# Performance work log

Hardware: AMD Instinct MI355X
Metric: run time of the kernel (lower is better)

The kernel has to match this reference:

```python
import jax, jax.numpy as jnp
import numpy as np

D_MODEL = 1024
D_HEAD = 64
M_BITS = 32


def setup_inputs() -> dict:
    key = jax.random.key(0)
    ks = jax.random.split(key, 6)
    B, N, M = 2, 2048, 2048
    Q = jax.random.normal(ks[0], (B, N, D_MODEL), dtype=jnp.float32)
    K = jax.random.normal(ks[1], (B, M, D_MODEL), dtype=jnp.float32)
    V = jax.random.normal(ks[2], (B, M, D_MODEL), dtype=jnp.float32)
    s = 1.0 / np.sqrt(D_MODEL)
    Wq = jax.random.normal(ks[3], (D_MODEL, M_BITS), dtype=jnp.float32) * s
    Wk = jax.random.normal(ks[4], (D_MODEL, M_BITS), dtype=jnp.float32) * s
    Wv = jax.random.normal(ks[5], (D_MODEL, D_HEAD), dtype=jnp.float32) * s
    temperature = jnp.ones((1,), dtype=jnp.float32)
    return {"Q": Q, "K": K, "V": V, "Wq": Wq, "Wk": Wk, "Wv": Wv,
            "temperature": temperature}


def tropical_matmul(A, Bt):
    # A: [B, N, m], Bt: [B, M, m] (already transposed form of [B, m, M])
    # (A \odot B)_{ij} = min_k (A_ik + B_kj)
    return jnp.min(A[:, :, None, :] + Bt[:, None, :, :], axis=-1)  # [B, N, M]


def reference(Q, K, V, Wq, Wk, Wv, temperature):
    # REWA tropical encoders (continuous): linear projections to m_bits
    Qt = jnp.einsum('bnd,dm->bnm', Q, Wq)   # [B, N, m_bits]
    Kt = jnp.einsum('bsd,dm->bsm', K, Wk)   # [B, M, m_bits]
    Vp = jnp.einsum('bsd,dh->bsh', V, Wv)   # [B, M, d_head]
    # tropical (min-plus) scores, negated so shorter paths score higher
    scores = -tropical_matmul(Qt, Kt)       # [B, N, M]
    scores = scores / jax.nn.softplus(temperature[0])
    attn = jax.nn.softmax(scores, axis=-1)  # [B, N, M]
    out = jnp.einsum('bnm,bmh->bnh', attn, Vp)  # [B, N, d_head]
    return out, attn
```

## Files before the change

kernel.cpp:

```cpp
#include <hip/hip_runtime.h>
#include <math.h>

#define DM 1024
#define NB 2048
#define MBITS 32
#define DH 64

typedef __attribute__((ext_vector_type(4))) float floatx4;
typedef __attribute__((ext_vector_type(8))) short shortx8;

__device__ __forceinline__ unsigned short f32_to_bf16(float f) {
    union { float f; unsigned u; } v; v.f = f;
    unsigned r = v.u + 0x7FFF + ((v.u >> 16) & 1);
    return (unsigned short)(r >> 16);
}

__device__ __forceinline__ void split2(float x0, float x1, unsigned& hp, unsigned& lp) {
    union { float f; unsigned u; } a, b; a.f = x0; b.f = x1;
    unsigned h0 = a.u & 0xFFFF0000u, h1 = b.u & 0xFFFF0000u;
    union { unsigned u; float f; } hf0, hf1; hf0.u = h0; hf1.u = h1;
    union { float f; unsigned u; } c, d;
    c.f = x0 - hf0.f;
    d.f = x1 - hf1.f;
    hp = (h0 >> 16) | h1;
    lp = (c.u >> 16) | (d.u & 0xFFFF0000u);
}

__global__ __launch_bounds__(256) void wprep_kernel(
    const float* __restrict__ Wq, const float* __restrict__ Wk,
    const float* __restrict__ Wv, unsigned short* __restrict__ Wf)
{
    int wv = blockIdx.x * 4 + (threadIdx.x >> 6);
    int l  = threadIdx.x & 63;
    const float* W; int C, kc32, ct;
    if (wv < 64)       { W = Wq; C = 32; kc32 = wv >> 1;  ct = wv & 1; }
    else if (wv < 128) { W = Wk; C = 32; int z = wv - 64;  kc32 = z >> 1; ct = z & 1; }
    else               { W = Wv; C = 64; int z = wv - 128; kc32 = z >> 2; ct = z & 3; }
    int k0 = kc32 * 32 + (l >> 4) * 8;
    int c  = ct * 16 + (l & 15);
    float x[8];
    #pragma unroll
    for (int j = 0; j < 8; ++j) x[j] = W[(size_t)(k0 + j) * C + c];
    unsigned hp[4], lp[4];
    #pragma unroll
    for (int j2 = 0; j2 < 4; ++j2) split2(x[2 * j2], x[2 * j2 + 1], hp[j2], lp[j2]);
    uint4 hv; hv.x = hp[0]; hv.y = hp[1]; hv.z = hp[2]; hv.w = hp[3];
    uint4 lv; lv.x = lp[0]; lv.y = lp[1]; lv.z = lp[2]; lv.w = lp[3];
    *(uint4*)&Wf[(size_t)wv * 1024 + l * 8]       = hv;
    *(uint4*)&Wf[(size_t)wv * 1024 + 512 + l * 8] = lv;
}

__global__ __launch_bounds__(256) void proj_mfma2_kernel(
    const float* __restrict__ Q, const float* __restrict__ K, const float* __restrict__ V,
    const unsigned short* __restrict__ Wf,
    float* __restrict__ Qt, float* __restrict__ KtT, unsigned short* __restrict__ VpT)
{
    __shared__ float red[4][64][16];

    int gb = blockIdx.x;
    int job = gb >> 8, tile = gb & 255;
    int r0 = tile * 16;
    const float* X = (job == 0) ? Q : (job == 1) ? K : V;
    int ntct  = (job == 2) ? 4 : 2;
    int pbase = job << 6;
    int t = threadIdx.x, w = t >> 6, l = t & 63;
    int lrow = l & 15, lq = l >> 4;

    const float* xrow = &X[(size_t)(r0 + lrow) * DM + w * 256 + lq * 8];

    floatx4 acc[4];
    #pragma unroll
    for (int i = 0; i < 4; ++i) acc[i] = (floatx4){0.f, 0.f, 0.f, 0.f};

    #pragma unroll
    for (int s = 0; s < 8; ++s) {
        floatx4 g0 = *(const floatx4*)(xrow + s * 32);
        floatx4 g1 = *(const floatx4*)(xrow + s * 32 + 4);
        union { unsigned u[4]; shortx8 v; } ahi, alo;
        split2(g0.x, g0.y, ahi.u[0], alo.u[0]);
        split2(g0.z, g0.w, ahi.u[1], alo.u[1]);
        split2(g1.x, g1.y, ahi.u[2], alo.u[2]);
        split2(g1.z, g1.w, ahi.u[3], alo.u[3]);
        int kc32 = w * 8 + s;
        #pragma unroll
        for (int ct = 0; ct < 4; ++ct) {
            if (ct >= ntct) break;
            int p = pbase + kc32 * ntct + ct;
            const unsigned short* wp = &Wf[(size_t)p * 1024 + l * 8];
            shortx8 bhi = *(const shortx8*)wp;
            shortx8 blo = *(const shortx8*)(wp + 512);
            acc[ct] = __builtin_amdgcn_mfma_f32_16x16x32_bf16(ahi.v, bhi, acc[ct], 0, 0, 0);
            acc[ct] = __builtin_amdgcn_mfma_f32_16x16x32_bf16(ahi.v, blo, acc[ct], 0, 0, 0);
            acc[ct] = __builtin_amdgcn_mfma_f32_16x16x32_bf16(alo.v, bhi, acc[ct], 0, 0, 0);
        }
    }

    #pragma unroll
    for (int ct = 0; ct < 4; ++ct) {
        if (ct >= ntct) break;
        #pragma unroll
        for (int r = 0; r < 4; ++r) red[w][l][ct * 4 + r] = acc[ct][r];
    }
    __syncthreads();

    int row = r0 + lq * 4 + w;
    if (job == 0) {
        #pragma unroll
        for (int ct = 0; ct < 2; ++ct) {
            float v = red[0][l][ct * 4 + w] + red[1][l][ct * 4 + w]
                    + red[2][l][ct * 4 + w] + red[3][l][ct * 4 + w];
            Qt[(size_t)row * MBITS + ct * 16 + lrow] = v;
        }
    } else if (job == 1) {
        int bb = row >> 11, j = row & 2047;
        #pragma unroll
        for (int ct = 0; ct < 2; ++ct) {
            float v = red[0][l][ct * 4 + w] + red[1][l][ct * 4 + w]
                    + red[2][l][ct * 4 + w] + red[3][l][ct * 4 + w];
            KtT[(size_t)bb * (MBITS * NB) + (size_t)(ct * 16 + lrow) * NB + j] = v;
        }
    } else {
        int bb = row >> 11, j = row & 2047;
        #pragma unroll
        for (int ct = 0; ct < 4; ++ct) {
            float v = red[0][l][ct * 4 + w] + red[1][l][ct * 4 + w]
                    + red[2][l][ct * 4 + w] + red[3][l][ct * 4 + w];
            VpT[(size_t)bb * (DH * NB) + (size_t)(ct * 16 + lrow) * NB + j] = f32_to_bf16(v);
        }
    }
}

__global__ __launch_bounds__(1024) void fused_score_out_kernel(
    const float* __restrict__ Qt, const float* __restrict__ KtT,
    const unsigned short* __restrict__ VpT, const float* __restrict__ temp,
    float* __restrict__ outp, float* __restrict__ attn)
{
    __shared__ unsigned short Elds[16][2056];
    __shared__ float redsum2[16][2];
    __shared__ float redC[12][64][4];

    const int b  = blockIdx.y;
    const int i0 = blockIdx.x * 8;
    const int t  = threadIdx.x;
    const int w  = t >> 6, l = t & 63;

    {
        uint4 z; z.x = 0; z.y = 0; z.z = 0; z.w = 0;
        uint4* base = (uint4*)&Elds[8][0];
        for (int zi = t; zi < 2056; zi += 1024) base[zi] = z;
    }

    const float tv = temp[0];
    const float c2 = -(1.0f / log1pf(__expf(tv))) * 1.44269504088896340736f;

    {
        const int ip  = w & 3;
        const int jqb = (w >> 2) * 512;
        const int p   = l >> 4;
        const int l16 = l & 15;

        const float* Qbase = &Qt[(size_t)(b * NB + i0 + ip * 2) * MBITS + p * 8];
        floatx4 qa0 = *(const floatx4*)(Qbase);
        floatx4 qa1 = *(const floatx4*)(Qbase + 4);
        floatx4 qb0 = *(const floatx4*)(Qbase + MBITS);
        floatx4 qb1 = *(const floatx4*)(Qbase + MBITS + 4);

        const float* Kp = &KtT[(size_t)b * (MBITS * NB) + (size_t)(p * 8) * NB];
        float sacc0 = 0.f, sacc1 = 0.f;

        #pragma unroll 1
        for (int s = 0; s < 4; ++s) {
            const int j0 = jqb + s * 128 + l16 * 8;
            float m0[8], m1[8];
            #pragma unroll
            for (int jj = 0; jj < 8; ++jj) { m0[jj] = 1e30f; m1[jj] = 1e30f; }

            #pragma unroll
            for (int kp = 0; kp < 8; ++kp) {
                const float* kr = Kp + (size_t)kp * NB + j0;
                floatx4 k0 = *(const floatx4*)kr;
                floatx4 k1 = *(const floatx4*)(kr + 4);
                float qa = (kp < 4) ? qa0[kp] : qa1[kp - 4];
                float qb = (kp < 4) ? qb0[kp] : qb1[kp - 4];
                float kv[8] = {k0.x, k0.y, k0.z, k0.w, k1.x, k1.y, k1.z, k1.w};
                #pragma unroll
                for (int jj = 0; jj < 8; ++jj) {
                    m0[jj] = fminf(m0[jj], qa + kv[jj]);
                    m1[jj] = fminf(m1[jj], qb + kv[jj]);
                }
            }
            #pragma unroll
            for (int jj = 0; jj < 8; ++jj) {
                m0[jj] = fminf(m0[jj], __shfl_xor(m0[jj], 16, 64));
                m0[jj] = fminf(m0[jj], __shfl_xor(m0[jj], 32, 64));
                m1[jj] = fminf(m1[jj], __shfl_xor(m1[jj], 16, 64));
                m1[jj] = fminf(m1[jj], __shfl_xor(m1[jj], 32, 64));
            }
            float e0[8], e1[8];
            #pragma unroll
            for (int jj = 0; jj < 8; ++jj) {
                e0[jj] = exp2f(c2 * m0[jj]);
                e1[jj] = exp2f(c2 * m1[jj]);
            }
            uint4 u0, u1;
            u0.x = (unsigned)f32_to_bf16(e0[0]) | ((unsigned)f32_to_bf16(e0[1]) << 16);
            u0.y = (unsigned)f32_to_bf16(e0[2]) | ((unsigned)f32_to_bf16(e0[3]) << 16);
            u0.z = (unsigned)f32_to_bf16(e0[4]) | ((unsigned)f32_to_bf16(e0[5]) << 16);
            u0.w = (unsigned)f32_to_bf16(e0[6]) | ((unsigned)f32_to_bf16(e0[7]) << 16);
            u1.x = (unsigned)f32_to_bf16(e1[0]) | ((unsigned)f32_to_bf16(e1[1]) << 16);
            u1.y = (unsigned)f32_to_bf16(e1[2]) | ((unsigned)f32_to_bf16(e1[3]) << 16);
            u1.z = (unsigned)f32_to_bf16(e1[4]) | ((unsigned)f32_to_bf16(e1[5]) << 16);
            u1.w = (unsigned)f32_to_bf16(e1[6]) | ((unsigned)f32_to_bf16(e1[7]) << 16);
            if (l < 16) {
                *(uint4*)&Elds[ip * 2][j0]     = u0;
                *(uint4*)&Elds[ip * 2 + 1][j0] = u1;
            }
            float s0 = ((e0[0] + e0[1]) + (e0[2] + e0[3])) + ((e0[4] + e0[5]) + (e0[6] + e0[7]));
            float s1 = ((e1[0] + e1[1]) + (e1[2] + e1[3])) + ((e1[4] + e1[5]) + (e1[6] + e1[7]));
            #pragma unroll
            for (int off = 1; off < 16; off <<= 1) {
                s0 += __shfl_xor(s0, off, 64);
                s1 += __shfl_xor(s1, off, 64);
            }
            sacc0 += s0; sacc1 += s1;
        }
        if (l == 0) { redsum2[w][0] = sacc0; redsum2[w][1] = sacc1; }
    }
    __syncthreads();

    const int mrow = l & 15, q4 = l >> 4;
    const int hh  = (w & 3) * 16 + mrow;
    const int kg  = w >> 2;
    floatx4 acc = {0.f, 0.f, 0.f, 0.f};
    const unsigned short* Vb = &VpT[(size_t)b * (DH * NB) + (size_t)hh * NB];

    #pragma unroll
    for (int jc2 = 0; jc2 < 8; ++jc2) {
        #pragma unroll
        for (int t2 = 0; t2 < 2; ++t2) {
            int ks = kg * 2 + t2;
            int joff = jc2 * 256 + ks * 32 + q4 * 8;
            shortx8 a  = *(const shortx8*)&Elds[mrow][joff];
            shortx8 bf = *(const shortx8*)&Vb[joff];
            acc = __builtin_amdgcn_mfma_f32_16x16x32_bf16(a, bf, acc, 0, 0, 0);
        }
    }

    {
        const int rw = w & 7, jh = w >> 3, rp = rw >> 1, rq = rw & 1;
        float iv = 1.0f / ((redsum2[rp][rq] + redsum2[4 + rp][rq])
                         + (redsum2[8 + rp][rq] + redsum2[12 + rp][rq]));
        #pragma unroll
        for (int u = 0; u < 4; ++u) {
            int j = jh * 1024 + u * 256 + l * 4;
            uint2 pk = *(const uint2*)&Elds[rw][j];
            union { unsigned u; float f; } x0, x1, x2, x3;
            x0.u = pk.x << 16; x1.u = pk.x & 0xFFFF0000u;
            x2.u = pk.y << 16; x3.u = pk.y & 0xFFFF0000u;
            floatx4 o;
            o.x = x0.f * iv; o.y = x1.f * iv; o.z = x2.f * iv; o.w = x3.f * iv;
            *(floatx4*)&attn[(size_t)(b * NB + i0 + rw) * 2048 + j] = o;
        }
    }

    if (w >= 4) *(floatx4*)&redC[w - 4][l][0] = acc;
    __syncthreads();
    if (w < 4) {
        floatx4 v0 = *(const floatx4*)&redC[w][l][0];
        floatx4 v1 = *(const floatx4*)&redC[w + 4][l][0];
        floatx4 v2 = *(const floatx4*)&redC[w + 8][l][0];
        if (l < 32) {
            #pragma unroll
            for (int r = 0; r < 4; ++r) {
                int irow = q4 * 4 + r;
                int rp = irow >> 1, rq = irow & 1;
                float ivr = 1.0f / ((redsum2[rp][rq] + redsum2[4 + rp][rq])
                                  + (redsum2[8 + rp][rq] + redsum2[12 + rp][rq]));
                float v = ((acc[r] + v0[r]) + (v1[r] + v2[r]));
                outp[(size_t)(b * NB + i0 + irow) * DH + w * 16 + mrow] = v * ivr;
            }
        }
    }
}

extern "C" void kernel_launch(void* const* d_in, const int* in_sizes, int n_in,
                              void* d_out, int out_size, void* d_ws, size_t ws_size,
                              hipStream_t stream) {
    (void)in_sizes; (void)n_in; (void)out_size; (void)ws_size;
    const float* Q    = (const float*)d_in[0];
    const float* K    = (const float*)d_in[1];
    const float* V    = (const float*)d_in[2];
    const float* Wq   = (const float*)d_in[3];
    const float* Wk   = (const float*)d_in[4];
    const float* Wv   = (const float*)d_in[5];
    const float* temp = (const float*)d_in[6];

    float* outp = (float*)d_out;
    float* attn = outp + 2 * 2048 * 64;

    char* ws = (char*)d_ws;
    float*          Qt  = (float*)(ws);
    float*          KtT = (float*)(ws + 524288);
    unsigned short* Wf  = (unsigned short*)(ws + 1179648);
    unsigned short* VpT = (unsigned short*)(ws + 1703936);

    wprep_kernel<<<64, 256, 0, stream>>>(Wq, Wk, Wv, Wf);
    proj_mfma2_kernel<<<768, 256, 0, stream>>>(Q, K, V, Wf, Qt, KtT, VpT);
    fused_score_out_kernel<<<dim3(256, 2), 1024, 0, stream>>>(Qt, KtT, VpT, temp, outp, attn);
}
```

Measured before the change: 161.7 us.

## Process 16 query rows per block and reuse Elds for output reduction

```diff
diff --git a/kernel.cpp b/kernel.cpp
--- a/kernel.cpp
+++ b/kernel.cpp
@@ -130,32 +130,26 @@
     }
 }
 
-__global__ __launch_bounds__(1024) void fused_score_out_kernel(
+__global__ __attribute__((amdgpu_waves_per_eu(8))) __launch_bounds__(1024)
+void fused_score_out_kernel(
     const float* __restrict__ Qt, const float* __restrict__ KtT,
     const unsigned short* __restrict__ VpT, const float* __restrict__ temp,
     float* __restrict__ outp, float* __restrict__ attn)
 {
     __shared__ unsigned short Elds[16][2056];
     __shared__ float redsum2[16][2];
-    __shared__ float redC[12][64][4];
 
     const int b  = blockIdx.y;
-    const int i0 = blockIdx.x * 8;
+    const int i0 = blockIdx.x * 16;
     const int t  = threadIdx.x;
     const int w  = t >> 6, l = t & 63;
 
-    {
-        uint4 z; z.x = 0; z.y = 0; z.z = 0; z.w = 0;
-        uint4* base = (uint4*)&Elds[8][0];
-        for (int zi = t; zi < 2056; zi += 1024) base[zi] = z;
-    }
-
     const float tv = temp[0];
     const float c2 = -(1.0f / log1pf(__expf(tv))) * 1.44269504088896340736f;
 
     {
-        const int ip  = w & 3;
-        const int jqb = (w >> 2) * 512;
+        const int ip  = w & 7;
+        const int jhb = (w >> 3) * 1024;
         const int p   = l >> 4;
         const int l16 = l & 15;
 
@@ -169,8 +163,8 @@
         float sacc0 = 0.f, sacc1 = 0.f;
 
         #pragma unroll 1
-        for (int s = 0; s < 4; ++s) {
-            const int j0 = jqb + s * 128 + l16 * 8;
+        for (int s = 0; s < 8; ++s) {
+            const int j0 = jhb + s * 128 + l16 * 8;
             float m0[8], m1[8];
             #pragma unroll
             for (int jj = 0; jj < 8; ++jj) { m0[jj] = 1e30f; m1[jj] = 1e30f; }
@@ -247,38 +241,35 @@
     }
 
     {
-        const int rw = w & 7, jh = w >> 3, rp = rw >> 1, rq = rw & 1;
-        float iv = 1.0f / ((redsum2[rp][rq] + redsum2[4 + rp][rq])
-                         + (redsum2[8 + rp][rq] + redsum2[12 + rp][rq]));
-        #pragma unroll
-        for (int u = 0; u < 4; ++u) {
-            int j = jh * 1024 + u * 256 + l * 4;
-            uint2 pk = *(const uint2*)&Elds[rw][j];
+        float iv = 1.0f / (redsum2[w >> 1][w & 1] + redsum2[8 + (w >> 1)][w & 1]);
+        #pragma unroll
+        for (int u = 0; u < 8; ++u) {
+            int j = u * 256 + l * 4;
+            uint2 pk = *(const uint2*)&Elds[w][j];
             union { unsigned u; float f; } x0, x1, x2, x3;
             x0.u = pk.x << 16; x1.u = pk.x & 0xFFFF0000u;
             x2.u = pk.y << 16; x3.u = pk.y & 0xFFFF0000u;
             floatx4 o;
             o.x = x0.f * iv; o.y = x1.f * iv; o.z = x2.f * iv; o.w = x3.f * iv;
-            *(floatx4*)&attn[(size_t)(b * NB + i0 + rw) * 2048 + j] = o;
-        }
-    }
-
-    if (w >= 4) *(floatx4*)&redC[w - 4][l][0] = acc;
+            *(floatx4*)&attn[(size_t)(b * NB + i0 + w) * 2048 + j] = o;
+        }
+    }
+    __syncthreads();
+
+    float* redCf = (float*)&Elds[0][0];
+    if (w >= 4) *(floatx4*)&redCf[(((w - 4) * 64) + l) * 4] = acc;
     __syncthreads();
     if (w < 4) {
-        floatx4 v0 = *(const floatx4*)&redC[w][l][0];
-        floatx4 v1 = *(const floatx4*)&redC[w + 4][l][0];
-        floatx4 v2 = *(const floatx4*)&redC[w + 8][l][0];
-        if (l < 32) {
-            #pragma unroll
-            for (int r = 0; r < 4; ++r) {
-                int irow = q4 * 4 + r;
-                int rp = irow >> 1, rq = irow & 1;
-                float ivr = 1.0f / ((redsum2[rp][rq] + redsum2[4 + rp][rq])
-                                  + (redsum2[8 + rp][rq] + redsum2[12 + rp][rq]));
-                float v = ((acc[r] + v0[r]) + (v1[r] + v2[r]));
-                outp[(size_t)(b * NB + i0 + irow) * DH + w * 16 + mrow] = v * ivr;
-            }
+        floatx4 v0 = *(const floatx4*)&redCf[((w * 64) + l) * 4];
+        floatx4 v1 = *(const floatx4*)&redCf[(((w + 4) * 64) + l) * 4];
+        floatx4 v2 = *(const floatx4*)&redCf[(((w + 8) * 64) + l) * 4];
+        #pragma unroll
+        for (int r = 0; r < 4; ++r) {
+            int irow = q4 * 4 + r;
+            float ivr = 1.0f / (redsum2[irow >> 1][irow & 1]
+                              + redsum2[8 + (irow >> 1)][irow & 1]);
+            float v = ((acc[r] + v0[r]) + (v1[r] + v2[r]));
+            outp[(size_t)(b * NB + i0 + irow) * DH + w * 16 + mrow] = v * ivr;
         }
     }
 }
@@ -306,5 +297,5 @@
 
     wprep_kernel<<<64, 256, 0, stream>>>(Wq, Wk, Wv, Wf);
     proj_mfma2_kernel<<<768, 256, 0, stream>>>(Q, K, V, Wf, Qt, KtT, VpT);
-    fused_score_out_kernel<<<dim3(256, 2), 1024, 0, stream>>>(Qt, KtT, VpT, temp, outp, attn);
-}
+    fused_score_out_kernel<<<dim3(128, 2), 1024, 0, stream>>>(Qt, KtT, VpT, temp, outp, attn);
+}
```

After: 176.7 us. 1.09x slower.
